# Optimization experiments

Hardware: AMD Instinct MI355X
Metric: run time of the kernel (lower is better)

## Reference

```python
import jax, jax.numpy as jnp
import numpy as np
import math

B, N, E = 4, 20000, 320000
CIN, SD, CF, TF = 4, 2, 8, 4
W, L, S, H, FFN, OUT = 256, 4, 64, 8, 1024, 4
D = W // H
EPS = 1e-6  # graph_bias_eps


def _layer_norm(x, w, b):
    mu = jnp.mean(x, -1, keepdims=True)
    var = jnp.mean((x - mu) ** 2, -1, keepdims=True)
    return (x - mu) * jax.lax.rsqrt(var + 1e-5) * w + b


def _aggregate(row, col, vals, x):
    # sparse adj (N,N) @ x per batch: y[b,i] = sum_e vals[e] * x[b, col[e]] for row[e]==i
    def one(xb):
        return jax.ops.segment_sum(vals[:, None] * xb[col], row, num_segments=N)
    return jax.vmap(one)(x)


def setup_inputs() -> dict:
    key = jax.random.key(0)
    ks = jax.random.split(key, 24)
    def n(i, shape, scale=0.02):
        return jax.random.normal(ks[i], shape, dtype=jnp.float32) * scale
    inp = {}
    inp['fields'] = jax.random.normal(ks[0], (B, N, CIN), dtype=jnp.float32)
    inp['coords'] = jax.random.uniform(ks[1], (B, N, SD), dtype=jnp.float32)
    inp['t_norm'] = jax.random.uniform(ks[2], (B,), dtype=jnp.float32)
    inp['adj_values'] = jax.random.uniform(ks[3], (E,), dtype=jnp.float32)
    # --- parameters ---
    inp['freq_matrix'] = jax.random.normal(ks[4], (SD, CF), dtype=jnp.float32)
    inp['omega'] = 1000.0 ** (-jnp.arange(TF, dtype=jnp.float32) / TF)
    inp['in_w'] = n(5, (CIN + 2 * CF + 2 * TF, W)); inp['in_b'] = jnp.zeros((W,), jnp.float32)
    inp['ln1_w'] = jnp.ones((L, W), jnp.float32); inp['ln1_b'] = jnp.zeros((L, W), jnp.float32)
    inp['ln2_w'] = jnp.ones((L, W), jnp.float32); inp['ln2_b'] = jnp.zeros((L, W), jnp.float32)
    inp['slice_w'] = n(6, (L, W, S)); inp['slice_b'] = jnp.zeros((L, S), jnp.float32)
    inp['q_w'] = n(7, (L, W, W)); inp['q_b'] = jnp.zeros((L, W), jnp.float32)
    inp['k_w'] = n(8, (L, W, W)); inp['k_b'] = jnp.zeros((L, W), jnp.float32)
    inp['v_w'] = n(9, (L, W, W)); inp['v_b'] = jnp.zeros((L, W), jnp.float32)
    inp['o_w'] = n(10, (L, W, W)); inp['o_b'] = jnp.zeros((L, W), jnp.float32)
    inp['beta_raw'] = jnp.full((L,), math.log(math.expm1(0.13)), jnp.float32)
    inp['ffn1_w'] = n(11, (L, W, FFN)); inp['ffn1_b'] = jnp.zeros((L, FFN), jnp.float32)
    inp['ffn2_w'] = n(12, (L, FFN, W)); inp['ffn2_b'] = jnp.zeros((L, W), jnp.float32)
    inp['out_w'] = n(13, (W, OUT)); inp['out_b'] = jnp.zeros((OUT,), jnp.float32)
    inp['adj_indices'] = jax.random.randint(ks[14], (2, E), 0, N, dtype=jnp.int32)
    return inp


def reference(fields, coords, t_norm, adj_values, freq_matrix, omega, in_w, in_b,
              ln1_w, ln1_b, ln2_w, ln2_b, slice_w, slice_b, q_w, q_b, k_w, k_b,
              v_w, v_b, o_w, o_b, beta_raw, ffn1_w, ffn1_b, ffn2_w, ffn2_b,
              out_w, out_b, adj_indices):
    row, col = adj_indices[0], adj_indices[1]
    # spatial + temporal encoders
    sp = 2.0 * jnp.pi * (coords @ freq_matrix)
    spat = jnp.concatenate([jnp.sin(sp), jnp.cos(sp)], -1)               # (B,N,2*CF)
    ang = (t_norm * 1000.0)[:, None] * omega[None, :]
    temb = jnp.concatenate([jnp.sin(ang), jnp.cos(ang)], -1)             # (B,2*TF)
    temb = jnp.broadcast_to(temb[:, None, :], (B, N, 2 * TF))
    h = jnp.concatenate([fields, spat, temb], -1) @ in_w + in_b          # (B,N,W)
    for l in range(L):
        # ---- GraphBiasAttention on norm1(h) ----
        hn = _layer_norm(h, ln1_w[l], ln1_b[l])
        weights = jax.nn.softmax(hn @ slice_w[l] + slice_b[l], -1)       # (B,N,S)
        wsum = jnp.maximum(weights.sum(1), EPS)                          # (B,S)
        slices = jnp.einsum('bns,bnc->bsc', weights, hn) / wsum[..., None]
        gw = _aggregate(row, col, adj_values, weights)                   # (B,N,S)
        gb = jnp.einsum('bns,bnt->bst', weights, gw)                     # (B,S,S)
        gb = 0.5 * (gb + gb.transpose(0, 2, 1))
        gb = gb / jnp.maximum(gb.sum(-1, keepdims=True), EPS)
        gb = jnp.log(jnp.maximum(gb, EPS))
        q = (slices @ q_w[l] + q_b[l]).reshape(B, S, H, D).transpose(0, 2, 1, 3)
        k = (slices @ k_w[l] + k_b[l]).reshape(B, S, H, D).transpose(0, 2, 1, 3)
        v = (slices @ v_w[l] + v_b[l]).reshape(B, S, H, D).transpose(0, 2, 1, 3)
        logits = jnp.einsum('bhsd,bhtd->bhst', q, k) / math.sqrt(D)
        logits = logits + jax.nn.softplus(beta_raw[l]) * gb[:, None]
        attn = jax.nn.softmax(logits, -1)
        so = jnp.einsum('bhst,bhtd->bhsd', attn, v).transpose(0, 2, 1, 3).reshape(B, S, W)
        so = so @ o_w[l] + o_b[l]
        h = h + jnp.einsum('bns,bsc->bnc', weights, so)
        # ---- FFN ----
        hn2 = _layer_norm(h, ln2_w[l], ln2_b[l])
        h = h + (jax.nn.gelu(hn2 @ ffn1_w[l] + ffn1_b[l], approximate=False) @ ffn2_w[l] + ffn2_b[l])
    return h @ out_w + out_b                                             # (B,N,OUT)
```

## Files before the change

kernel.cpp:

```cpp
#include <hip/hip_runtime.h>
#include <math.h>

#define BB 4
#define NN 20000
#define NE 320000
#define WW 256
#define SS 64
#define NH 8
#define HD 32
#define NF 1024
#define NL 4
#define GEPS 1e-6f

typedef __attribute__((ext_vector_type(8))) short short8v;
typedef __attribute__((ext_vector_type(4))) float f32x4;

static __device__ __forceinline__ short f2bf(float x){
  union { float f; unsigned u; } v; v.f = x;
  unsigned r = v.u + 0x7fffu + ((v.u >> 16) & 1u);
  return (short)(r >> 16);
}
static __device__ __forceinline__ float bfu_lo(unsigned u){
  union { unsigned u; float f; } v; v.u = u << 16; return v.f;
}
static __device__ __forceinline__ float bfu_hi(unsigned u){
  union { unsigned u; float f; } v; v.u = u & 0xffff0000u; return v.f;
}
static __device__ __forceinline__ float gelu_f(float x){
  return 0.5f*x*(1.0f + erff(x*0.70710678118654752f));
}

#define GLOAD16(gsrc, ldst) \
  __builtin_amdgcn_global_load_lds( \
      (const __attribute__((address_space(1))) void*)(gsrc), \
      (__attribute__((address_space(3))) void*)(ldst), 16, 0, 0)

__global__ __launch_bounds__(256) void k_embed(
    const float* __restrict__ fields, const float* __restrict__ coords,
    const float* __restrict__ t_norm, const float* __restrict__ freq,
    const float* __restrict__ omega, const float* __restrict__ in_w,
    const float* __restrict__ in_b, float* __restrict__ h)
{
  __shared__ float inv[16][28];
  __shared__ float temb[8];
  const int t = threadIdx.x;
  const size_t tok0 = (size_t)blockIdx.x * 16;
  const int b = (int)(tok0 / NN);
  if (t < 8) {
    int f = t & 3;
    float ang = t_norm[b] * 1000.0f * omega[f];
    temb[t] = (t < 4) ? sinf(ang) : cosf(ang);
  }
  if (t < 128) {
    int tok = t >> 3, f = t & 7;
    size_t n = tok0 + tok;
    float c0 = coords[n*2+0], c1 = coords[n*2+1];
    float sp = 6.283185307179586f * (c0*freq[f] + c1*freq[8+f]);
    inv[tok][4+f]  = sinf(sp);
    inv[tok][12+f] = cosf(sp);
  } else if (t < 192) {
    int idx = t - 128; int tok = idx >> 2, i = idx & 3;
    inv[tok][i] = fields[(tok0+tok)*4 + i];
  }
  __syncthreads();
  if (t < 128) {
    int tok = t >> 3, f = t & 7;
    inv[tok][20+f] = temb[f];
  }
  __syncthreads();
  float acc[16];
  float bias = in_b[t];
  #pragma unroll
  for (int i = 0; i < 16; i++) acc[i] = bias;
  #pragma unroll 4
  for (int k = 0; k < 28; k++) {
    float w = in_w[k*WW + t];
    #pragma unroll
    for (int i = 0; i < 16; i++) acc[i] += inv[i][k]*w;
  }
  #pragma unroll
  for (int i = 0; i < 16; i++) h[(tok0+i)*WW + t] = acc[i];
}

__global__ __launch_bounds__(256) void k_lnw(
    const float* __restrict__ h, const float* __restrict__ lnw,
    const float* __restrict__ lnb, const float* __restrict__ sw,
    const float* __restrict__ sb, float* __restrict__ wts,
    short* __restrict__ wtsb, float* __restrict__ mu_rstd)
{
  __shared__ float hn[16][WW];
  __shared__ float ps[16][16], pq[16][16];
  __shared__ float mus[16], rss[16];
  const int t = threadIdx.x;
  const size_t tok0 = (size_t)blockIdx.x * 16;
  const int tok = t >> 4, seg = t & 15;
  {
    const float4* hp = (const float4*)(h + (tok0+tok)*WW + seg*16);
    float sum = 0.f, sq = 0.f;
    #pragma unroll
    for (int i = 0; i < 4; i++){
      float4 v = hp[i];
      sum += v.x+v.y+v.z+v.w;
      sq  += v.x*v.x+v.y*v.y+v.z*v.z+v.w*v.w;
      *((float4*)&hn[tok][seg*16 + i*4]) = v;
    }
    ps[tok][seg] = sum; pq[tok][seg] = sq;
  }
  __syncthreads();
  if (t < 16){
    float s0=0.f, q0=0.f;
    #pragma unroll
    for (int i = 0; i < 16; i++){ s0 += ps[t][i]; q0 += pq[t][i]; }
    float mu = s0*(1.0f/WW);
    float var = q0*(1.0f/WW) - mu*mu;
    float rs = rsqrtf(var + 1e-5f);
    mus[t] = mu; rss[t] = rs;
    mu_rstd[(tok0 + t)*2]     = mu;
    mu_rstd[(tok0 + t)*2 + 1] = rs;
  }
  __syncthreads();
  {
    float mu = mus[tok], rs = rss[tok];
    #pragma unroll
    for (int i = 0; i < 16; i++){
      int c = seg*16 + i;
      hn[tok][c] = (hn[tok][c]-mu)*rs*lnw[c] + lnb[c];
    }
  }
  __syncthreads();
  const int s = t & 63, tg = t >> 6;
  float acc[4];
  float bs = sb[s];
  #pragma unroll
  for (int i = 0; i < 4; i++) acc[i] = bs;
  for (int c4 = 0; c4 < 64; c4++){
    float w0 = sw[(c4*4+0)*SS + s];
    float w1 = sw[(c4*4+1)*SS + s];
    float w2 = sw[(c4*4+2)*SS + s];
    float w3 = sw[(c4*4+3)*SS + s];
    #pragma unroll
    for (int i = 0; i < 4; i++){
      float4 hv = *((const float4*)&hn[tg*4+i][c4*4]);
      acc[i] += hv.x*w0 + hv.y*w1 + hv.z*w2 + hv.w*w3;
    }
  }
  #pragma unroll
  for (int i = 0; i < 4; i++){
    float m = acc[i];
    #pragma unroll
    for (int off = 32; off > 0; off >>= 1) m = fmaxf(m, __shfl_xor(m, off));
    float e = expf(acc[i] - m);
    float ssum = e;
    #pragma unroll
    for (int off = 32; off > 0; off >>= 1) ssum += __shfl_xor(ssum, off);
    float wv = e/ssum;
    wts[(tok0 + tg*4 + i)*SS + s] = wv;
    wtsb[(tok0 + tg*4 + i)*SS + s] = f2bf(wv);
  }
}

__global__ __launch_bounds__(256) void k_slices(
    const float* __restrict__ h, const float* __restrict__ wts,
    const float* __restrict__ mu_rstd, const float* __restrict__ lnw,
    const float* __restrict__ lnb, float* __restrict__ sacc,
    float* __restrict__ wsum)
{
  __shared__ float wstage[16][SS];
  const int t = threadIdx.x;
  const int b = blockIdx.y;
  const int n0 = blockIdx.x * 128;
  const float lw = lnw[t], lb = lnb[t];
  float acc[SS];
  #pragma unroll
  for (int s = 0; s < SS; s++) acc[s] = 0.f;
  float wsl = 0.f;
  for (int it = 0; it < 8; it++){
    int nb = n0 + it*16;
    {
      int tk = t >> 4, s4 = (t & 15)*4;
      int n = nb + tk;
      float4 v = make_float4(0.f,0.f,0.f,0.f);
      if (n < NN) v = *((const float4*)(wts + ((size_t)b*NN + n)*SS + s4));
      *((float4*)&wstage[tk][s4]) = v;
    }
    __syncthreads();
    #pragma unroll 4
    for (int tk = 0; tk < 16; tk++){
      int n = nb + tk;
      if (n < NN){
        size_t g = (size_t)b*NN + n;
        float mu = mu_rstd[g*2], rsd = mu_rstd[g*2+1];
        float hv = h[g*WW + t];
        float hnv = (hv-mu)*rsd*lw + lb;
        #pragma unroll
        for (int s4 = 0; s4 < 16; s4++){
          float4 wv = *((const float4*)&wstage[tk][s4*4]);
          acc[s4*4+0] += wv.x*hnv;
          acc[s4*4+1] += wv.y*hnv;
          acc[s4*4+2] += wv.z*hnv;
          acc[s4*4+3] += wv.w*hnv;
        }
      }
    }
    if (t < SS){
      #pragma unroll
      for (int tk = 0; tk < 16; tk++) wsl += wstage[tk][t];
    }
    __syncthreads();
  }
  #pragma unroll
  for (int s = 0; s < SS; s++)
    atomicAdd(&sacc[((size_t)b*SS + s)*WW + t], acc[s]);
  if (t < SS) atomicAdd(&wsum[b*SS + t], wsl);
}

__global__ __launch_bounds__(256) void k_slices_fin(
    const float* __restrict__ sacc, const float* __restrict__ wsum,
    float* __restrict__ slices)
{
  int i = blockIdx.x*256 + threadIdx.x;
  int sidx = i >> 8;
  float ws = fmaxf(wsum[sidx], GEPS);
  slices[i] = sacc[i] / ws;
}

#define GB_BLKS 1000
#define GB_PB   250
#define GB_EDG  (NE/GB_PB)
__global__ __launch_bounds__(256) void k_gb2(
    const short* __restrict__ wtsb, const int* __restrict__ adj,
    const float* __restrict__ vals, float* __restrict__ gb)
{
  __shared__ float gbw[SS*SS];
  const int t = threadIdx.x;
  const int bid = blockIdx.x;
  const int xcd = bid & 7;
  const int b = xcd >> 1;
  const int grp = (bid >> 3)*2 + (xcd & 1);
  const int e0 = grp * GB_EDG;
  const int w = t >> 6, l = t & 63;
  const int sg = l >> 3, tg = l & 7;
  #pragma unroll
  for (int i = 0; i < 16; i++) gbw[t + 256*i] = 0.f;
  __syncthreads();
  float acc[8][8];
  #pragma unroll
  for (int i = 0; i < 8; i++)
    #pragma unroll
    for (int u = 0; u < 8; u++) acc[i][u] = 0.f;
  const short* wb = wtsb + (size_t)b*NN*SS;
  for (int e = e0 + w; e < e0 + GB_EDG; e += 8){
    int row0 = adj[e],     col0 = adj[NE + e];
    int row1 = adj[e + 4], col1 = adj[NE + e + 4];
    float v0 = vals[e], v1 = vals[e + 4];
    uint4 ru0 = *(const uint4*)(wb + (size_t)row0*SS + sg*8);
    uint4 cu0 = *(const uint4*)(wb + (size_t)col0*SS + tg*8);
    uint4 ru1 = *(const uint4*)(wb + (size_t)row1*SS + sg*8);
    uint4 cu1 = *(const uint4*)(wb + (size_t)col1*SS + tg*8);
    float rr[8], cc[8];
    rr[0]=bfu_lo(ru0.x)*v0; rr[1]=bfu_hi(ru0.x)*v0;
    rr[2]=bfu_lo(ru0.y)*v0; rr[3]=bfu_hi(ru0.y)*v0;
    rr[4]=bfu_lo(ru0.z)*v0; rr[5]=bfu_hi(ru0.z)*v0;
    rr[6]=bfu_lo(ru0.w)*v0; rr[7]=bfu_hi(ru0.w)*v0;
    cc[0]=bfu_lo(cu0.x); cc[1]=bfu_hi(cu0.x);
    cc[2]=bfu_lo(cu0.y); cc[3]=bfu_hi(cu0.y);
    cc[4]=bfu_lo(cu0.z); cc[5]=bfu_hi(cu0.z);
    cc[6]=bfu_lo(cu0.w); cc[7]=bfu_hi(cu0.w);
    #pragma unroll
    for (int i = 0; i < 8; i++)
      #pragma unroll
      for (int u = 0; u < 8; u++) acc[i][u] += rr[i]*cc[u];
    rr[0]=bfu_lo(ru1.x)*v1; rr[1]=bfu_hi(ru1.x)*v1;
    rr[2]=bfu_lo(ru1.y)*v1; rr[3]=bfu_hi(ru1.y)*v1;
    rr[4]=bfu_lo(ru1.z)*v1; rr[5]=bfu_hi(ru1.z)*v1;
    rr[6]=bfu_lo(ru1.w)*v1; rr[7]=bfu_hi(ru1.w)*v1;
    cc[0]=bfu_lo(cu1.x); cc[1]=bfu_hi(cu1.x);
    cc[2]=bfu_lo(cu1.y); cc[3]=bfu_hi(cu1.y);
    cc[4]=bfu_lo(cu1.z); cc[5]=bfu_hi(cu1.z);
    cc[6]=bfu_lo(cu1.w); cc[7]=bfu_hi(cu1.w);
    #pragma unroll
    for (int i = 0; i < 8; i++)
      #pragma unroll
      for (int u = 0; u < 8; u++) acc[i][u] += rr[i]*cc[u];
  }
  #pragma unroll
  for (int i = 0; i < 8; i++)
    #pragma unroll
    for (int u = 0; u < 8; u++)
      atomicAdd(&gbw[(sg*8+i)*SS + tg*8 + u], acc[i][u]);
  __syncthreads();
  #pragma unroll
  for (int i = 0; i < 16; i++){
    int idx = t + 256*i;
    atomicAdd(&gb[(size_t)b*SS*SS + idx], gbw[idx]);
  }
}

__global__ __launch_bounds__(256) void k_gbfin(
    const float* __restrict__ gbin, float* __restrict__ gbout,
    const float* __restrict__ beta_raw, int layer)
{
  __shared__ float g[SS*SS];
  __shared__ float gs[SS*SS];
  __shared__ float rs[SS];
  const int t = threadIdx.x;
  const int b = blockIdx.x;
  #pragma unroll
  for (int i = 0; i < 16; i++) g[t + 256*i] = gbin[(size_t)b*SS*SS + t + 256*i];
  __syncthreads();
  #pragma unroll
  for (int i = 0; i < 16; i++){
    int idx = t + 256*i; int r = idx >> 6, c = idx & 63;
    gs[idx] = 0.5f*(g[idx] + g[c*SS + r]);
  }
  __syncthreads();
  if (t < SS){
    float sum = 0.f;
    for (int c = 0; c < SS; c++) sum += gs[t*SS + c];
    rs[t] = 1.0f / fmaxf(sum, GEPS);
  }
  __syncthreads();
  float beta = log1pf(expf(beta_raw[layer]));
  #pragma unroll
  for (int i = 0; i < 16; i++){
    int idx = t + 256*i; int r = idx >> 6;
    gbout[(size_t)b*SS*SS + idx] = beta * logf(fmaxf(gs[idx]*rs[r], GEPS));
  }
}

__global__ __launch_bounds__(256) void k_attn(
    const float* __restrict__ slices,
    const float* __restrict__ qw, const float* __restrict__ qb,
    const float* __restrict__ kw, const float* __restrict__ kb,
    const float* __restrict__ vw, const float* __restrict__ vb,
    const float* __restrict__ gbf, float* __restrict__ so)
{
  __shared__ float sl[SS][WW];
  __shared__ float qh[SS][HD], kh[SS][HD], vh[SS][HD];
  __shared__ float att[SS][SS];
  const int t = threadIdx.x;
  const int hh = blockIdx.x, b = blockIdx.y;
  {
    const float4* sp4 = (const float4*)(slices + (size_t)b*SS*WW);
    float4* sl4 = (float4*)sl;
    #pragma unroll
    for (int i = 0; i < 16; i++) sl4[t + 256*i] = sp4[t + 256*i];
  }
  __syncthreads();
  const int s = t >> 2, dq = t & 3, d0 = dq*8;
  float aq[8], ak[8], av[8];
  #pragma unroll
  for (int j = 0; j < 8; j++){
    aq[j] = qb[hh*HD + d0 + j];
    ak[j] = kb[hh*HD + d0 + j];
    av[j] = vb[hh*HD + d0 + j];
  }
  for (int c = 0; c < WW; c++){
    float sv = sl[s][c];
    const float4* q4 = (const float4*)(qw + (size_t)c*WW + hh*HD + d0);
    const float4* k4 = (const float4*)(kw + (size_t)c*WW + hh*HD + d0);
    const float4* v4 = (const float4*)(vw + (size_t)c*WW + hh*HD + d0);
    float4 qa = q4[0], qc = q4[1];
    float4 ka = k4[0], kc = k4[1];
    float4 va = v4[0], vc = v4[1];
    aq[0]+=sv*qa.x; aq[1]+=sv*qa.y; aq[2]+=sv*qa.z; aq[3]+=sv*qa.w;
    aq[4]+=sv*qc.x; aq[5]+=sv*qc.y; aq[6]+=sv*qc.z; aq[7]+=sv*qc.w;
    ak[0]+=sv*ka.x; ak[1]+=sv*ka.y; ak[2]+=sv*ka.z; ak[3]+=sv*ka.w;
    ak[4]+=sv*kc.x; ak[5]+=sv*kc.y; ak[6]+=sv*kc.z; ak[7]+=sv*kc.w;
    av[0]+=sv*va.x; av[1]+=sv*va.y; av[2]+=sv*va.z; av[3]+=sv*va.w;
    av[4]+=sv*vc.x; av[5]+=sv*vc.y; av[6]+=sv*vc.z; av[7]+=sv*vc.w;
  }
  *((float4*)&qh[s][d0])   = make_float4(aq[0],aq[1],aq[2],aq[3]);
  *((float4*)&qh[s][d0+4]) = make_float4(aq[4],aq[5],aq[6],aq[7]);
  *((float4*)&kh[s][d0])   = make_float4(ak[0],ak[1],ak[2],ak[3]);
  *((float4*)&kh[s][d0+4]) = make_float4(ak[4],ak[5],ak[6],ak[7]);
  *((float4*)&vh[s][d0])   = make_float4(av[0],av[1],av[2],av[3]);
  *((float4*)&vh[s][d0+4]) = make_float4(av[4],av[5],av[6],av[7]);
  __syncthreads();
  float qreg[HD];
  #pragma unroll
  for (int d4 = 0; d4 < 8; d4++){
    float4 qv = *((const float4*)&qh[s][d4*4]);
    qreg[d4*4+0]=qv.x; qreg[d4*4+1]=qv.y; qreg[d4*4+2]=qv.z; qreg[d4*4+3]=qv.w;
  }
  const int tc0 = dq*16;
  float lg[16];
  #pragma unroll
  for (int u = 0; u < 16; u++){
    float a = 0.f;
    #pragma unroll
    for (int d4 = 0; d4 < 8; d4++){
      float4 kv = *((const float4*)&kh[tc0+u][d4*4]);
      a += qreg[d4*4+0]*kv.x + qreg[d4*4+1]*kv.y + qreg[d4*4+2]*kv.z + qreg[d4*4+3]*kv.w;
    }
    lg[u] = a*0.17677669529663687f + gbf[((size_t)b*SS + s)*SS + tc0 + u];
  }
  float m = lg[0];
  #pragma unroll
  for (int u = 1; u < 16; u++) m = fmaxf(m, lg[u]);
  m = fmaxf(m, __shfl_xor(m, 1));
  m = fmaxf(m, __shfl_xor(m, 2));
  float ssum = 0.f;
  #pragma unroll
  for (int u = 0; u < 16; u++){ lg[u] = expf(lg[u]-m); ssum += lg[u]; }
  ssum += __shfl_xor(ssum, 1);
  ssum += __shfl_xor(ssum, 2);
  float invs = 1.0f/ssum;
  #pragma unroll
  for (int u = 0; u < 16; u++) att[s][tc0+u] = lg[u]*invs;
  __syncthreads();
  float ao[8];
  #pragma unroll
  for (int j = 0; j < 8; j++) ao[j] = 0.f;
  for (int t2 = 0; t2 < SS; t2++){
    float a = att[s][t2];
    float4 v0 = *((const float4*)&vh[t2][d0]);
    float4 v1 = *((const float4*)&vh[t2][d0+4]);
    ao[0]+=a*v0.x; ao[1]+=a*v0.y; ao[2]+=a*v0.z; ao[3]+=a*v0.w;
    ao[4]+=a*v1.x; ao[5]+=a*v1.y; ao[6]+=a*v1.z; ao[7]+=a*v1.w;
  }
  float* sop = so + ((size_t)b*SS + s)*WW + hh*HD + d0;
  *((float4*)sop)     = make_float4(ao[0],ao[1],ao[2],ao[3]);
  *((float4*)(sop+4)) = make_float4(ao[4],ao[5],ao[6],ao[7]);
}

__global__ __launch_bounds__(256) void k_oproj(
    const float* __restrict__ so, const float* __restrict__ ow,
    const float* __restrict__ ob, float* __restrict__ so_out)
{
  __shared__ float st[16][WW];
  const int t = threadIdx.x;
  const int b = blockIdx.y;
  const int s0 = blockIdx.x * 16;
  {
    const float4* sp = (const float4*)(so + ((size_t)b*SS + s0)*WW);
    float4* st4 = (float4*)st;
    #pragma unroll
    for (int i = 0; i < 4; i++) st4[t + 256*i] = sp[t + 256*i];
  }
  __syncthreads();
  float acc[16];
  float bias = ob[t];
  #pragma unroll
  for (int i = 0; i < 16; i++) acc[i] = bias;
  for (int k4 = 0; k4 < 64; k4++){
    float w0 = ow[(size_t)(k4*4+0)*WW + t];
    float w1 = ow[(size_t)(k4*4+1)*WW + t];
    float w2 = ow[(size_t)(k4*4+2)*WW + t];
    float w3 = ow[(size_t)(k4*4+3)*WW + t];
    #pragma unroll
    for (int i = 0; i < 16; i++){
      float4 sv = *((const float4*)&st[i][k4*4]);
      acc[i] += sv.x*w0 + sv.y*w1 + sv.z*w2 + sv.w*w3;
    }
  }
  #pragma unroll
  for (int i = 0; i < 16; i++)
    so_out[((size_t)b*SS + s0 + i)*WW + t] = acc[i];
}

__global__ __launch_bounds__(256) void k_tr1(
    const float* __restrict__ in, short* __restrict__ out)
{
  __shared__ float tile[32][33];
  const int tx = threadIdx.x & 31;
  const int ty = threadIdx.x >> 5;
  const size_t moff = (size_t)blockIdx.z * WW * NF;
  const int x = blockIdx.x*32 + tx;
  const int y0 = blockIdx.y*32;
  #pragma unroll
  for (int i = 0; i < 4; i++){
    int r = y0 + ty + i*8;
    tile[ty + i*8][tx] = in[moff + (size_t)r*NF + x];
  }
  __syncthreads();
  const int k = y0 + tx;
  #pragma unroll
  for (int i = 0; i < 4; i++){
    int j = blockIdx.x*32 + ty + i*8;
    int off = j*WW + ((((k>>3) ^ (j&7)))<<3) + (k&7);
    out[moff + off] = f2bf(tile[tx][ty + i*8]);
  }
}

__global__ __launch_bounds__(256) void k_tr2(
    const float* __restrict__ in, short* __restrict__ out)
{
  __shared__ float tile[32][33];
  const int tx = threadIdx.x & 31;
  const int ty = threadIdx.x >> 5;
  const size_t moff = (size_t)blockIdx.z * NF * WW;
  const int x = blockIdx.x*32 + tx;
  const int y0 = blockIdx.y*32;
  #pragma unroll
  for (int i = 0; i < 4; i++){
    int r = y0 + ty + i*8;
    tile[ty + i*8][tx] = in[moff + (size_t)r*WW + x];
  }
  __syncthreads();
  const int ch = y0 >> 5;
  const int jl = tx;
  #pragma unroll
  for (int i = 0; i < 4; i++){
    int c = blockIdx.x*32 + ty + i*8;
    int off = ch*8192 + c*32 + ((((jl>>3) ^ (c&3)))<<3) + (jl&7);
    out[moff + off] = f2bf(tile[tx][ty + i*8]);
  }
}

#define FTM 64
#define CH 32
__global__ __launch_bounds__(256, 4) void k_ffn8(
    float* __restrict__ h, const float* __restrict__ wts,
    const float* __restrict__ so_out,
    const float* __restrict__ lnw, const float* __restrict__ lnb,
    const short* __restrict__ w1t, const float* __restrict__ b1,
    const short* __restrict__ w2t, const float* __restrict__ b2)
{
  __shared__ __align__(16) char wbig[32768];
  __align__(16) __shared__ short gbuf[4][16*40];
  short* w1s = (short*)wbig;
  short* w2s = (short*)(wbig + 16384);
  float* sob = (float*)wbig;
  const int t = threadIdx.x;
  const int w = t >> 6, l = t & 63;
  const int lm = l & 15, g = l >> 4;
  const int b = blockIdx.y;
  const int ltok0 = blockIdx.x * FTM;
  const bool valid = (ltok0 + w*16) < NN;
  const int lA = valid ? (ltok0 + w*16 + lm) : lm;
  const size_t tokA = (size_t)b*NN + lA;
  float* hrow = h + tokA*WW;
  const float* wrow = wts + tokA*SS;

  float sum = 0.f, sq = 0.f;
  #pragma unroll
  for (int half = 0; half < 2; half++){
    __syncthreads();
    #pragma unroll
    for (int it = 0; it < 8; it++){
      int idx = it*256 + t;
      int s = idx >> 5, c4 = (idx & 31) << 2;
      GLOAD16(so_out + ((size_t)b*SS + s)*WW + half*128 + c4,
              ((float*)sob) + (size_t)idx*4);
    }
    __syncthreads();
    float4 hv[8], upd[8];
    #pragma unroll
    for (int u = 0; u < 8; u++){
      hv[u] = *(const float4*)(hrow + (half*4 + (u>>1))*32 + g*8 + (u&1)*4);
      upd[u] = make_float4(0.f,0.f,0.f,0.f);
    }
    #pragma unroll 2
    for (int s4 = 0; s4 < 16; s4++){
      float4 wv4 = *(const float4*)(wrow + s4*4);
      #pragma unroll
      for (int k = 0; k < 4; k++){
        float wv = (k==0)?wv4.x:(k==1)?wv4.y:(k==2)?wv4.z:wv4.w;
        const float* sor = sob + (s4*4+k)*128 + g*8;
        #pragma unroll
        for (int u = 0; u < 8; u++){
          float4 so4 = *(const float4*)(sor + (u>>1)*32 + (u&1)*4);
          upd[u].x += wv*so4.x; upd[u].y += wv*so4.y;
          upd[u].z += wv*so4.z; upd[u].w += wv*so4.w;
        }
      }
    }
    #pragma unroll
    for (int u = 0; u < 8; u++){
      float4 nv;
      nv.x = hv[u].x + upd[u].x; nv.y = hv[u].y + upd[u].y;
      nv.z = hv[u].z + upd[u].z; nv.w = hv[u].w + upd[u].w;
      sum += nv.x+nv.y+nv.z+nv.w;
      sq  += nv.x*nv.x+nv.y*nv.y+nv.z*nv.z+nv.w*nv.w;
      if (valid)
        *(float4*)(hrow + (half*4 + (u>>1))*32 + g*8 + (u&1)*4) = nv;
    }
  }
  sum += __shfl_xor(sum, 16); sum += __shfl_xor(sum, 32);
  sq  += __shfl_xor(sq, 16);  sq  += __shfl_xor(sq, 32);
  float mu = sum*(1.0f/WW);
  float var = sq*(1.0f/WW) - mu*mu;
  float rs = rsqrtf(var + 1e-5f);
  short8v hn[8];
  #pragma unroll
  for (int f = 0; f < 8; f++){
    float4 a  = *(const float4*)(hrow + f*32 + g*8);
    float4 bq = *(const float4*)(hrow + f*32 + g*8 + 4);
    float4 w0 = *(const float4*)(lnw + f*32 + g*8);
    float4 w1 = *(const float4*)(lnw + f*32 + g*8 + 4);
    float4 b0 = *(const float4*)(lnb + f*32 + g*8);
    float4 b1v = *(const float4*)(lnb + f*32 + g*8 + 4);
    short8v fr;
    fr[0] = f2bf((a.x -mu)*rs*w0.x + b0.x);
    fr[1] = f2bf((a.y -mu)*rs*w0.y + b0.y);
    fr[2] = f2bf((a.z -mu)*rs*w0.z + b0.z);
    fr[3] = f2bf((a.w -mu)*rs*w0.w + b0.w);
    fr[4] = f2bf((bq.x-mu)*rs*w1.x + b1v.x);
    fr[5] = f2bf((bq.y-mu)*rs*w1.y + b1v.y);
    fr[6] = f2bf((bq.z-mu)*rs*w1.z + b1v.z);
    fr[7] = f2bf((bq.w-mu)*rs*w1.w + b1v.w);
    hn[f] = fr;
  }
  f32x4 acc2[16];
  #pragma unroll
  for (int ct = 0; ct < 16; ct++)
    acc2[ct] = (f32x4){0.f,0.f,0.f,0.f};
  __syncthreads();

  for (int ch = 0; ch < NF/CH; ch++){
    const int j0 = ch*CH;
    const short* w1c = w1t + (size_t)j0*256;
    const short* w2c = w2t + (size_t)ch*8192;
    #pragma unroll
    for (int it = 0; it < 4; it++){
      int p = w*4 + it;
      GLOAD16(w1c + p*512 + l*8, w1s + p*512);
      GLOAD16(w2c + p*512 + l*8, w2s + p*512);
    }
    __syncthreads();
    #pragma unroll
    for (int jt = 0; jt < 2; jt++){
      f32x4 d0 = (f32x4){0.f,0.f,0.f,0.f};
      const int rl = jt*16 + lm;
      #pragma unroll
      for (int ks = 0; ks < 8; ks++){
        short8v af = *(const short8v*)(w1s + rl*256 + ((((ks<<2)|g) ^ (rl&7))<<3));
        d0 = __builtin_amdgcn_mfma_f32_16x16x32_bf16(af, hn[ks], d0, 0, 0, 0);
      }
      float4 bb = *(const float4*)(b1 + j0 + jt*16 + g*4);
      float x0 = gelu_f(d0[0] + bb.x), x1 = gelu_f(d0[1] + bb.y);
      float x2 = gelu_f(d0[2] + bb.z), x3 = gelu_f(d0[3] + bb.w);
      unsigned u0 = (unsigned)(unsigned short)f2bf(x0) | ((unsigned)(unsigned short)f2bf(x1) << 16);
      unsigned u1 = (unsigned)(unsigned short)f2bf(x2) | ((unsigned)(unsigned short)f2bf(x3) << 16);
      *(uint2*)(&gbuf[w][lm*40 + jt*16 + g*4]) = make_uint2(u0, u1);
    }
    short8v gA0 = *(const short8v*)(&gbuf[w][lm*40 + g*8]);
    #pragma unroll
    for (int ct = 0; ct < 16; ct++){
      const int row = ct*16 + lm;
      short8v a0 = *(const short8v*)(w2s + row*32 + (((g ^ (row&3)))<<3));
      acc2[ct] = __builtin_amdgcn_mfma_f32_16x16x32_bf16(a0, gA0, acc2[ct], 0, 0, 0);
    }
    __syncthreads();
  }
  if (valid){
    float* tb = (float*)&gbuf[w][0];
    const int tok_l = l >> 2, cq = (l & 3)*4;
    const size_t trow = (size_t)b*NN + ltok0 + w*16;
    #pragma unroll
    for (int ct = 0; ct < 16; ct++){
      float4 sv;
      sv.x = acc2[ct][0]; sv.y = acc2[ct][1];
      sv.z = acc2[ct][2]; sv.w = acc2[ct][3];
      *(float4*)(&tb[lm*20 + g*4]) = sv;
      float4 tv = *(const float4*)(&tb[tok_l*20 + cq]);
      float4 bb = *(const float4*)(b2 + ct*16 + cq);
      float* hp = h + (trow + tok_l)*WW + ct*16 + cq;
      float4 ho = *(const float4*)hp;
      ho.x += tv.x + bb.x; ho.y += tv.y + bb.y;
      ho.z += tv.z + bb.z; ho.w += tv.w + bb.w;
      *(float4*)hp = ho;
    }
  }
}

__global__ __launch_bounds__(256) void k_out(
    const float* __restrict__ h, const float* __restrict__ ow,
    const float* __restrict__ ob, float* __restrict__ out)
{
  size_t n = (size_t)blockIdx.x*256 + threadIdx.x;
  if (n >= (size_t)BB*NN) return;
  float a0=ob[0], a1=ob[1], a2=ob[2], a3=ob[3];
  const float4* hp = (const float4*)(h + n*WW);
  const float4* ow4 = (const float4*)ow;
  for (int c4 = 0; c4 < 64; c4++){
    float4 hv = hp[c4];
    float4 w0 = ow4[c4*4+0], w1 = ow4[c4*4+1], w2 = ow4[c4*4+2], w3 = ow4[c4*4+3];
    a0 += hv.x*w0.x + hv.y*w1.x + hv.z*w2.x + hv.w*w3.x;
    a1 += hv.x*w0.y + hv.y*w1.y + hv.z*w2.y + hv.w*w3.y;
    a2 += hv.x*w0.z + hv.y*w1.z + hv.z*w2.z + hv.w*w3.z;
    a3 += hv.x*w0.w + hv.y*w1.w + hv.z*w2.w + hv.w*w3.w;
  }
  *((float4*)(out + n*4)) = make_float4(a0,a1,a2,a3);
}

extern "C" void kernel_launch(void* const* d_in, const int* in_sizes, int n_in,
                              void* d_out, int out_size, void* d_ws, size_t ws_size,
                              hipStream_t stream) {
  const float* fields    = (const float*)d_in[0];
  const float* coords    = (const float*)d_in[1];
  const float* t_norm    = (const float*)d_in[2];
  const float* adj_vals  = (const float*)d_in[3];
  const float* freq      = (const float*)d_in[4];
  const float* omega     = (const float*)d_in[5];
  const float* in_w      = (const float*)d_in[6];
  const float* in_b      = (const float*)d_in[7];
  const float* ln1_w     = (const float*)d_in[8];
  const float* ln1_b     = (const float*)d_in[9];
  const float* ln2_w     = (const float*)d_in[10];
  const float* ln2_b     = (const float*)d_in[11];
  const float* slice_w   = (const float*)d_in[12];
  const float* slice_b   = (const float*)d_in[13];
  const float* q_w       = (const float*)d_in[14];
  const float* q_b       = (const float*)d_in[15];
  const float* k_w       = (const float*)d_in[16];
  const float* k_b       = (const float*)d_in[17];
  const float* v_w       = (const float*)d_in[18];
  const float* v_b       = (const float*)d_in[19];
  const float* o_w       = (const float*)d_in[20];
  const float* o_b       = (const float*)d_in[21];
  const float* beta_raw  = (const float*)d_in[22];
  const float* ffn1_w    = (const float*)d_in[23];
  const float* ffn1_b    = (const float*)d_in[24];
  const float* ffn2_w    = (const float*)d_in[25];
  const float* ffn2_b    = (const float*)d_in[26];
  const float* out_w     = (const float*)d_in[27];
  const float* out_b     = (const float*)d_in[28];
  const int*   adj       = (const int*)d_in[29];
  float* out = (float*)d_out;

  float* ws = (float*)d_ws;
  size_t off = 0;
  float* h        = ws + off; off += (size_t)BB*NN*WW;
  float* wts      = ws + off; off += (size_t)BB*NN*SS;
  float* mu_rstd  = ws + off; off += (size_t)BB*NN*2;
  float* sacc     = ws + off; off += (size_t)BB*SS*WW;
  float* wsumb    = ws + off; off += (size_t)BB*SS;
  float* gb       = ws + off; off += (size_t)BB*SS*SS;
  float* gbf      = ws + off; off += (size_t)BB*SS*SS;
  float* slices   = ws + off; off += (size_t)BB*SS*WW;
  float* so       = ws + off; off += (size_t)BB*SS*WW;
  float* so_out   = ws + off; off += (size_t)BB*SS*WW;
  short* w1tb     = (short*)(ws + off); off += (size_t)NL*WW*NF/2;
  short* w2tb     = (short*)(ws + off); off += (size_t)NL*WW*NF/2;
  short* wtsb     = (short*)(ws + off); off += (size_t)BB*NN*SS/2;

  hipLaunchKernelGGL(k_tr1, dim3(NF/32, WW/32, NL), dim3(256), 0, stream,
      ffn1_w, w1tb);
  hipLaunchKernelGGL(k_tr2, dim3(WW/32, NF/32, NL), dim3(256), 0, stream,
      ffn2_w, w2tb);

  hipLaunchKernelGGL(k_embed, dim3(BB*NN/16), dim3(256), 0, stream,
      fields, coords, t_norm, freq, omega, in_w, in_b, h);

  for (int l = 0; l < NL; l++){
    hipMemsetAsync(sacc, 0,
        (size_t)(BB*SS*WW + BB*SS + BB*SS*SS)*sizeof(float), stream);
    hipLaunchKernelGGL(k_lnw, dim3(BB*NN/16), dim3(256), 0, stream,
        h, ln1_w + l*WW, ln1_b + l*WW,
        slice_w + (size_t)l*WW*SS, slice_b + l*SS, wts, wtsb, mu_rstd);
    hipLaunchKernelGGL(k_slices, dim3(157, BB), dim3(256), 0, stream,
        h, wts, mu_rstd, ln1_w + l*WW, ln1_b + l*WW, sacc, wsumb);
    hipLaunchKernelGGL(k_slices_fin, dim3(BB*SS*WW/256), dim3(256), 0, stream,
        sacc, wsumb, slices);
    hipLaunchKernelGGL(k_gb2, dim3(GB_BLKS), dim3(256), 0, stream,
        wtsb, adj, adj_vals, gb);
    hipLaunchKernelGGL(k_gbfin, dim3(BB), dim3(256), 0, stream,
        gb, gbf, beta_raw, l);
    hipLaunchKernelGGL(k_attn, dim3(NH, BB), dim3(256), 0, stream,
        slices,
        q_w + (size_t)l*WW*WW, q_b + l*WW,
        k_w + (size_t)l*WW*WW, k_b + l*WW,
        v_w + (size_t)l*WW*WW, v_b + l*WW,
        gbf, so);
    hipLaunchKernelGGL(k_oproj, dim3(4, BB), dim3(256), 0, stream,
        so, o_w + (size_t)l*WW*WW, o_b + l*WW, so_out);
    hipLaunchKernelGGL(k_ffn8, dim3((NN + FTM - 1)/FTM, BB), dim3(256), 0, stream,
        h, wts, so_out, ln2_w + l*WW, ln2_b + l*WW,
        w1tb + (size_t)l*WW*NF, ffn1_b + l*NF,
        w2tb + (size_t)l*WW*NF, ffn2_b + l*WW);
  }

  hipLaunchKernelGGL(k_out, dim3((BB*NN + 255)/256), dim3(256), 0, stream,
      h, out_w, out_b, out);
}
```

Before: 3.129 ms.

## Fuse layernorm/slice-softmax kernel with slice accumulation kernel

Merges the LN1 + slice-weight softmax kernel with the slice accumulation kernel, so each block normalizes 128 tokens in groups of 16 and immediately accumulates weighted normalized features from shared memory. This avoids re-reading h and wts from global memory and drops the mu/rstd buffer and one launch. The cost is fewer blocks (157 per batch instead of 5000), which lowers parallelism for the projection/softmax phase, and more barriers per block.

```diff
diff --git a/kernel.cpp b/kernel.cpp
--- a/kernel.cpp
+++ b/kernel.cpp
@@ -82,124 +82,104 @@
   for (int i = 0; i < 16; i++) h[(tok0+i)*WW + t] = acc[i];
 }
 
-__global__ __launch_bounds__(256) void k_lnw(
+__global__ __launch_bounds__(256) void k_lnws(
     const float* __restrict__ h, const float* __restrict__ lnw,
     const float* __restrict__ lnb, const float* __restrict__ sw,
     const float* __restrict__ sb, float* __restrict__ wts,
-    short* __restrict__ wtsb, float* __restrict__ mu_rstd)
+    short* __restrict__ wtsb, float* __restrict__ sacc,
+    float* __restrict__ wsum)
 {
   __shared__ float hn[16][WW];
+  __shared__ float wstage[16][SS];
   __shared__ float ps[16][16], pq[16][16];
   __shared__ float mus[16], rss[16];
   const int t = threadIdx.x;
-  const size_t tok0 = (size_t)blockIdx.x * 16;
-  const int tok = t >> 4, seg = t & 15;
-  {
-    const float4* hp = (const float4*)(h + (tok0+tok)*WW + seg*16);
-    float sum = 0.f, sq = 0.f;
-    #pragma unroll
-    for (int i = 0; i < 4; i++){
-      float4 v = hp[i];
-      sum += v.x+v.y+v.z+v.w;
-      sq  += v.x*v.x+v.y*v.y+v.z*v.z+v.w*v.w;
-      *((float4*)&hn[tok][seg*16 + i*4]) = v;
-    }
-    ps[tok][seg] = sum; pq[tok][seg] = sq;
-  }
-  __syncthreads();
-  if (t < 16){
-    float s0=0.f, q0=0.f;
-    #pragma unroll
-    for (int i = 0; i < 16; i++){ s0 += ps[t][i]; q0 += pq[t][i]; }
-    float mu = s0*(1.0f/WW);
-    float var = q0*(1.0f/WW) - mu*mu;
-    float rs = rsqrtf(var + 1e-5f);
-    mus[t] = mu; rss[t] = rs;
-    mu_rstd[(tok0 + t)*2]     = mu;
-    mu_rstd[(tok0 + t)*2 + 1] = rs;
-  }
-  __syncthreads();
-  {
-    float mu = mus[tok], rs = rss[tok];
-    #pragma unroll
-    for (int i = 0; i < 16; i++){
-      int c = seg*16 + i;
-      hn[tok][c] = (hn[tok][c]-mu)*rs*lnw[c] + lnb[c];
-    }
-  }
-  __syncthreads();
-  const int s = t & 63, tg = t >> 6;
-  float acc[4];
-  float bs = sb[s];
-  #pragma unroll
-  for (int i = 0; i < 4; i++) acc[i] = bs;
-  for (int c4 = 0; c4 < 64; c4++){
-    float w0 = sw[(c4*4+0)*SS + s];
-    float w1 = sw[(c4*4+1)*SS + s];
-    float w2 = sw[(c4*4+2)*SS + s];
-    float w3 = sw[(c4*4+3)*SS + s];
-    #pragma unroll
-    for (int i = 0; i < 4; i++){
-      float4 hv = *((const float4*)&hn[tg*4+i][c4*4]);
-      acc[i] += hv.x*w0 + hv.y*w1 + hv.z*w2 + hv.w*w3;
-    }
-  }
-  #pragma unroll
-  for (int i = 0; i < 4; i++){
-    float m = acc[i];
-    #pragma unroll
-    for (int off = 32; off > 0; off >>= 1) m = fmaxf(m, __shfl_xor(m, off));
-    float e = expf(acc[i] - m);
-    float ssum = e;
-    #pragma unroll
-    for (int off = 32; off > 0; off >>= 1) ssum += __shfl_xor(ssum, off);
-    float wv = e/ssum;
-    wts[(tok0 + tg*4 + i)*SS + s] = wv;
-    wtsb[(tok0 + tg*4 + i)*SS + s] = f2bf(wv);
-  }
-}
-
-__global__ __launch_bounds__(256) void k_slices(
-    const float* __restrict__ h, const float* __restrict__ wts,
-    const float* __restrict__ mu_rstd, const float* __restrict__ lnw,
-    const float* __restrict__ lnb, float* __restrict__ sacc,
-    float* __restrict__ wsum)
-{
-  __shared__ float wstage[16][SS];
-  const int t = threadIdx.x;
   const int b = blockIdx.y;
   const int n0 = blockIdx.x * 128;
-  const float lw = lnw[t], lb = lnb[t];
+  const int tok = t >> 4, seg = t & 15;
+  const int s = t & 63, tg = t >> 6;
+  const float bs = sb[s];
   float acc[SS];
   #pragma unroll
-  for (int s = 0; s < SS; s++) acc[s] = 0.f;
+  for (int i = 0; i < SS; i++) acc[i] = 0.f;
   float wsl = 0.f;
-  for (int it = 0; it < 8; it++){
-    int nb = n0 + it*16;
+
+  for (int grp = 0; grp < 8; grp++){
+    const int nb = n0 + grp*16;
+    if (nb >= NN) break;
+    const size_t tok0 = (size_t)b*NN + nb;
     {
-      int tk = t >> 4, s4 = (t & 15)*4;
-      int n = nb + tk;
-      float4 v = make_float4(0.f,0.f,0.f,0.f);
-      if (n < NN) v = *((const float4*)(wts + ((size_t)b*NN + n)*SS + s4));
-      *((float4*)&wstage[tk][s4]) = v;
+      const float4* hp = (const float4*)(h + (tok0+tok)*WW + seg*16);
+      float sum = 0.f, sq = 0.f;
+      #pragma unroll
+      for (int i = 0; i < 4; i++){
+        float4 v = hp[i];
+        sum += v.x+v.y+v.z+v.w;
+        sq  += v.x*v.x+v.y*v.y+v.z*v.z+v.w*v.w;
+        *((float4*)&hn[tok][seg*16 + i*4]) = v;
+      }
+      ps[tok][seg] = sum; pq[tok][seg] = sq;
+    }
+    __syncthreads();
+    if (t < 16){
+      float s0=0.f, q0=0.f;
+      #pragma unroll
+      for (int i = 0; i < 16; i++){ s0 += ps[t][i]; q0 += pq[t][i]; }
+      float mu = s0*(1.0f/WW);
+      float var = q0*(1.0f/WW) - mu*mu;
+      mus[t] = mu; rss[t] = rsqrtf(var + 1e-5f);
+    }
+    __syncthreads();
+    {
+      float mu = mus[tok], rs = rss[tok];
+      #pragma unroll
+      for (int i = 0; i < 16; i++){
+        int c = seg*16 + i;
+        hn[tok][c] = (hn[tok][c]-mu)*rs*lnw[c] + lnb[c];
+      }
+    }
+    __syncthreads();
+    {
+      float a4[4];
+      #pragma unroll
+      for (int i = 0; i < 4; i++) a4[i] = bs;
+      for (int c4 = 0; c4 < 64; c4++){
+        float w0 = sw[(c4*4+0)*SS + s];
+        float w1 = sw[(c4*4+1)*SS + s];
+        float w2 = sw[(c4*4+2)*SS + s];
+        float w3 = sw[(c4*4+3)*SS + s];
+        #pragma unroll
+        for (int i = 0; i < 4; i++){
+          float4 hv = *((const float4*)&hn[tg*4+i][c4*4]);
+          a4[i] += hv.x*w0 + hv.y*w1 + hv.z*w2 + hv.w*w3;
+        }
+      }
+      #pragma unroll
+      for (int i = 0; i < 4; i++){
+        float m = a4[i];
+        #pragma unroll
+        for (int off = 32; off > 0; off >>= 1) m = fmaxf(m, __shfl_xor(m, off));
+        float e = expf(a4[i] - m);
+        float ssum = e;
+        #pragma unroll
+        for (int off = 32; off > 0; off >>= 1) ssum += __shfl_xor(ssum, off);
+        float wv = e/ssum;
+        wts[(tok0 + tg*4 + i)*SS + s]  = wv;
+        wtsb[(tok0 + tg*4 + i)*SS + s] = f2bf(wv);
+        wstage[tg*4+i][s] = wv;
+      }
     }
     __syncthreads();
     #pragma unroll 4
     for (int tk = 0; tk < 16; tk++){
-      int n = nb + tk;
-      if (n < NN){
-        size_t g = (size_t)b*NN + n;
-        float mu = mu_rstd[g*2], rsd = mu_rstd[g*2+1];
-        float hv = h[g*WW + t];
-        float hnv = (hv-mu)*rsd*lw + lb;
-        #pragma unroll
-        for (int s4 = 0; s4 < 16; s4++){
-          float4 wv = *((const float4*)&wstage[tk][s4*4]);
-          acc[s4*4+0] += wv.x*hnv;
-          acc[s4*4+1] += wv.y*hnv;
-          acc[s4*4+2] += wv.z*hnv;
-          acc[s4*4+3] += wv.w*hnv;
-        }
+      float hnv = hn[tk][t];
+      #pragma unroll
+      for (int s4 = 0; s4 < 16; s4++){
+        float4 wv = *((const float4*)&wstage[tk][s4*4]);
+        acc[s4*4+0] += wv.x*hnv;
+        acc[s4*4+1] += wv.y*hnv;
+        acc[s4*4+2] += wv.z*hnv;
+        acc[s4*4+3] += wv.w*hnv;
       }
     }
     if (t < SS){
@@ -209,8 +189,8 @@
     __syncthreads();
   }
   #pragma unroll
-  for (int s = 0; s < SS; s++)
-    atomicAdd(&sacc[((size_t)b*SS + s)*WW + t], acc[s]);
+  for (int i = 0; i < SS; i++)
+    atomicAdd(&sacc[((size_t)b*SS + i)*WW + t], acc[i]);
   if (t < SS) atomicAdd(&wsum[b*SS + t], wsl);
 }
 
@@ -724,7 +704,6 @@
   size_t off = 0;
   float* h        = ws + off; off += (size_t)BB*NN*WW;
   float* wts      = ws + off; off += (size_t)BB*NN*SS;
-  float* mu_rstd  = ws + off; off += (size_t)BB*NN*2;
   float* sacc     = ws + off; off += (size_t)BB*SS*WW;
   float* wsumb    = ws + off; off += (size_t)BB*SS;
   float* gb       = ws + off; off += (size_t)BB*SS*SS;
@@ -747,11 +726,9 @@
   for (int l = 0; l < NL; l++){
     hipMemsetAsync(sacc, 0,
         (size_t)(BB*SS*WW + BB*SS + BB*SS*SS)*sizeof(float), stream);
-    hipLaunchKernelGGL(k_lnw, dim3(BB*NN/16), dim3(256), 0, stream,
+    hipLaunchKernelGGL(k_lnws, dim3((NN + 127)/128, BB), dim3(256), 0, stream,
         h, ln1_w + l*WW, ln1_b + l*WW,
-        slice_w + (size_t)l*WW*SS, slice_b + l*SS, wts, wtsb, mu_rstd);
-    hipLaunchKernelGGL(k_slices, dim3(157, BB), dim3(256), 0, stream,
-        h, wts, mu_rstd, ln1_w + l*WW, ln1_b + l*WW, sacc, wsumb);
+        slice_w + (size_t)l*WW*SS, slice_b + l*SS, wts, wtsb, sacc, wsumb);
     hipLaunchKernelGGL(k_slices_fin, dim3(BB*SS*WW/256), dim3(256), 0, stream,
         sacc, wsumb, slices);
     hipLaunchKernelGGL(k_gb2, dim3(GB_BLKS), dim3(256), 0, stream,
```

After: 3.179 ms. No clear change (+1.6%).
